# Kernel tuning notes

Hardware: AMD Instinct MI355X
Metric: run time of the kernel (lower is better)

## Reference

```python
import jax, jax.numpy as jnp
import numpy as np

B, S, W, MODES, NUM, NLAYERS = 32, 8192, 128, 16, 8, 4
LG = 8192 + 40 - 1  # szie + len - 1 (Gabor filter length)
PI = float(np.pi)


def setup_inputs() -> dict:
    key = jax.random.key(0)
    ks = jax.random.split(key, 10)
    scale = 1.0 / (W * W)
    return {
        "x": jax.random.normal(ks[0], (B, S, 1), jnp.float32),
        "w1_re": scale * jax.random.uniform(ks[1], (NLAYERS, W, W, MODES), jnp.float32),
        "w1_im": scale * jax.random.uniform(ks[2], (NLAYERS, W, W, MODES), jnp.float32),
        "gamma": jnp.tile(jnp.linspace(0.01, 0.02, NUM, dtype=jnp.float32)[None], (NLAYERS, 1)),
        "fwhm": jnp.tile(jnp.linspace(0.001, 0.002, NUM, dtype=jnp.float32)[None], (NLAYERS, 1)),
        "w2": jax.random.uniform(ks[3], (NLAYERS, NUM), jnp.float32),
        "cw": jax.random.normal(ks[4], (NLAYERS, W, W), jnp.float32) / np.sqrt(W),
        "cb": jnp.zeros((NLAYERS, W), jnp.float32),
        "fc0_w": jax.random.normal(ks[5], (W, 2), jnp.float32) / np.sqrt(2.0),
        "fc0_b": jnp.zeros((W,), jnp.float32),
        "fc1_w": jax.random.normal(ks[6], (128, W), jnp.float32) / np.sqrt(W),
        "fc1_b": jnp.zeros((128,), jnp.float32),
        "fc2_w": jax.random.normal(ks[7], (1, 128), jnp.float32) / np.sqrt(128.0),
        "fc2_b": jnp.zeros((1,), jnp.float32),
    }


def _spectral_conv(h, w_re, w_im, gamma, fwhm, w2):
    # h: [B, C, S] real. w_re/w_im: [C, C, MODES]. gamma/fwhm/w2: [NUM].
    u = jnp.linspace(-0.5, 0.5, LG, dtype=h.dtype)                      # [LG]
    t1 = (gamma * PI / (fwhm + 1e-5))[:, None]                          # [NUM,1]
    gab = jnp.exp(-(t1 ** 2) * (u[None, :] - fwhm[:, None]) ** 2)       # [NUM,LG]
    gab = jnp.fft.ifftshift(gab, axes=-1)[:, :MODES]                     # [NUM,MODES]
    # weights2 is a scalar per latent kernel -> fold the num-reduction into an
    # effective per-mode Gabor weight (exact same math as the repeated einsum + sum).
    g_eff = jnp.einsum("k,km->m", w2, gab)                               # [MODES]
    w1 = (w_re + 1j * w_im) * g_eff[None, None, :]                       # [C,C,MODES] complex
    xf = jnp.fft.rfft(h)                                                 # [B,C,F], F=S//2+1
    out_m = jnp.einsum("bim,iom->bom", xf[..., :MODES], w1)              # [B,C,MODES]
    out = jnp.zeros(xf.shape, dtype=xf.dtype).at[..., :MODES].set(out_m)
    return jnp.fft.irfft(out, n=h.shape[-1])                             # [B,C,S]


def reference(x, w1_re, w1_im, gamma, fwhm, w2, cw, cb, fc0_w, fc0_b, fc1_w, fc1_b, fc2_w, fc2_b):
    b, s, _ = x.shape
    grid = jnp.broadcast_to(jnp.linspace(0.0, 1.0, s, dtype=x.dtype)[None, :, None], (b, s, 1))
    h = jnp.concatenate([x, grid], axis=-1)                              # [B,S,2]
    h = h @ fc0_w.T + fc0_b                                              # [B,S,W]
    h = jnp.transpose(h, (0, 2, 1))                                      # [B,W,S]
    for l in range(NLAYERS):
        x1 = _spectral_conv(h, w1_re[l], w1_im[l], gamma[l], fwhm[l], w2[l])
        x2 = jnp.einsum("oi,bis->bos", cw[l], h) + cb[l][None, :, None]  # 1x1 conv
        h = x1 + x2
        if l < NLAYERS - 1:
            h = jax.nn.gelu(h, approximate=False)
    h = jnp.transpose(h, (0, 2, 1))                                      # [B,S,W]
    h = jax.nn.gelu(h @ fc1_w.T + fc1_b, approximate=False)              # [B,S,128]
    return h @ fc2_w.T + fc2_b                                           # [B,S,1]
```

## Files before the change

### kernel.cpp

```cpp
#include <hip/hip_runtime.h>
#include <hip/hip_fp16.h>

#define BB 32
#define SS 8192
#define CC 128
#define MM 16
#define NUMK 8
#define NL 4

#define TWO_PI 6.2831853071795864769f

typedef _Float16 f16x8 __attribute__((ext_vector_type(8)));
typedef float f32x4 __attribute__((ext_vector_type(4)));

#define MFMA16(a, b, c) __builtin_amdgcn_mfma_f32_16x16x32_f16((a), (b), (c), 0, 0, 0)

__device__ __forceinline__ float gelu_f(float v) {
    float u = 0.7978845608f * fmaf(0.044715f * v * v, v, v);
    float a = fabsf(u);
    float e = __expf(-2.0f * a);
    float th = __fdividef(1.0f - e, 1.0f + e);
    th = copysignf(th, u);
    return 0.5f * v * (1.0f + th);
}

__device__ __align__(256) __half g_trigA[SS * 32];
__device__ __align__(256) __half g_trigD[32 * SS];
__device__ __align__(256) __half g_cwh[NL * CC * CC];
__device__ __align__(256) __half g_fc1h[CC * CC];
__device__ __align__(256) __half g_omh[BB * CC * 32];
__device__ __align__(256) float  g_Xfp[BB * 64 * 32 * CC];
__device__ __align__(256) float  g_Xf[BB * 32 * CC];
__device__ __align__(256) float  g_Xx[BB * MM * 2];
__device__ __align__(256) float  g_Xg[MM * 2];

__global__ __launch_bounds__(256) void k_prep(const float* __restrict__ cw,
                                              const float* __restrict__ fc1_w) {
    int idx = blockIdx.x * 256 + threadIdx.x;
    if (idx < NL * CC * CC) g_cwh[idx] = __float2half(cw[idx]);
    if (idx < CC * CC)      g_fc1h[idx] = __float2half(fc1_w[idx]);
}

__global__ __launch_bounds__(256) void k_trig() {
    int s = blockIdx.x * 256 + threadIdx.x;
    for (int m = 0; m < MM; m++) {
        int ms = (m * s) & (SS - 1);
        float th = (float)ms * (TWO_PI / (float)SS);
        float sn, cs;
        sincosf(th, &sn, &cs);
        g_trigA[s * 32 + m]        = __float2half(cs);
        g_trigA[s * 32 + 16 + m]   = __float2half(sn);
        g_trigD[m * SS + s]        = __float2half(cs);
        g_trigD[(16 + m) * SS + s] = __float2half(-sn);
    }
}

__global__ __launch_bounds__(256) void k_dftx(const float* __restrict__ x) {
    __shared__ float red[4][MM][2];
    int blk = blockIdx.x;
    int t = threadIdx.x;
    int lane = t & 63;
    int wv = t >> 6;

    float accR[MM], accI[MM], cr[MM], ci[MM], pc[MM], ps[MM];
#pragma unroll
    for (int m = 0; m < MM; m++) {
        float sn, cs;
        sincosf((TWO_PI / (float)SS) * (float)(m * t), &sn, &cs);
        cr[m] = cs; ci[m] = -sn;
        sincosf((TWO_PI * 256.0f / (float)SS) * (float)m, &sn, &cs);
        pc[m] = cs; ps[m] = -sn;
        accR[m] = 0.f; accI[m] = 0.f;
    }
    for (int k = 0; k < 32; k++) {
        int s = t + (k << 8);
        float v = (blk < BB) ? x[(blk << 13) + s] : (float)s * (1.0f / 8191.0f);
#pragma unroll
        for (int m = 0; m < MM; m++) {
            accR[m] = fmaf(v, cr[m], accR[m]);
            accI[m] = fmaf(v, ci[m], accI[m]);
            float nc = cr[m] * pc[m] - ci[m] * ps[m];
            float ns = cr[m] * ps[m] + ci[m] * pc[m];
            cr[m] = nc; ci[m] = ns;
        }
    }
#pragma unroll
    for (int m = 0; m < MM; m++) {
#pragma unroll
        for (int off = 32; off > 0; off >>= 1) {
            accR[m] += __shfl_xor(accR[m], off, 64);
            accI[m] += __shfl_xor(accI[m], off, 64);
        }
        if (lane == 0) { red[wv][m][0] = accR[m]; red[wv][m][1] = accI[m]; }
    }
    __syncthreads();
    if (t < MM * 2) {
        int m = t >> 1, p = t & 1;
        float s = red[0][m][p] + red[1][m][p] + red[2][m][p] + red[3][m][p];
        if (blk < BB) g_Xx[(blk << 5) + (m << 1) + p] = s;
        else          g_Xg[(m << 1) + p] = s;
    }
}

__global__ __launch_bounds__(256) void k_xf0(const float* __restrict__ fc0_w,
                                             const float* __restrict__ fc0_b) {
    int n = blockIdx.x * 256 + threadIdx.x;
    int i = n & 127, m2 = (n >> 7) & 31, b = n >> 12;
    int m = m2 & 15, p = m2 >> 4;
    float xv = g_Xx[(b << 5) + (m << 1) + p];
    float gv = g_Xg[(m << 1) + p];
    float v = fc0_w[2 * i] * xv + fc0_w[2 * i + 1] * gv;
    if (p == 0 && m == 0) v += (float)SS * fc0_b[i];
    g_Xf[(b << 12) + (m2 << 7) + i] = v;
}

__global__ __launch_bounds__(256) void k_fc0(const float* __restrict__ x,
                                             const float* __restrict__ fc0_w,
                                             const float* __restrict__ fc0_b,
                                             __half2* __restrict__ h2) {
    int idx = blockIdx.x * 256 + threadIdx.x;
    int w2i = idx & 63;
    int s = (idx >> 6) & (SS - 1);
    int b = idx >> 19;
    int w = w2i * 2;
    float g = (float)s * (1.0f / (float)(SS - 1));
    float xv = x[(b << 13) + s];
    float v0 = fmaf(fc0_w[2 * w], xv, fmaf(fc0_w[2 * w + 1], g, fc0_b[w]));
    float v1 = fmaf(fc0_w[2 * w + 2], xv, fmaf(fc0_w[2 * w + 3], g, fc0_b[w + 1]));
    h2[idx] = __floats2half2_rn(v0, v1);
}

__global__ __launch_bounds__(256) void k_red2() {
    int n = blockIdx.x * 256 + threadIdx.x;
    int i = n & 127, m2 = (n >> 7) & 31, b = n >> 12;
    const float* p = g_Xfp + (((b << 6) << 5) + (m2 << 7)) + i;
    float s = 0.f;
#pragma unroll 8
    for (int t = 0; t < 64; t++) s += p[t << 12];
    g_Xf[(b << 12) + (m2 << 7) + i] = s;
}

__global__ __launch_bounds__(256) void k_mix(const float* __restrict__ w1_re,
                                             const float* __restrict__ w1_im,
                                             const float* __restrict__ gamma,
                                             const float* __restrict__ fwhm,
                                             const float* __restrict__ w2,
                                             const float* __restrict__ cb, int l) {
    __shared__ float geff[MM];
    int t = threadIdx.x;
    if (t < MM) {
        float g = 0.f;
        for (int k = 0; k < NUMK; k++) {
            float fw = fwhm[l * NUMK + k];
            float t1 = gamma[l * NUMK + k] * 3.14159265358979f / (fw + 1e-5f);
            float u = (float)t * (1.0f / 8230.0f) - fw;
            g = fmaf(w2[l * NUMK + k], expf(-t1 * t1 * u * u), g);
        }
        geff[t] = g;
    }
    __syncthreads();

    int n = blockIdx.x * 256 + t;
    int m = n & 15, o = (n >> 4) & 127, b = n >> 11;
    const float* xr = g_Xf + (b << 12) + (m << 7);
    const float* xi = g_Xf + (b << 12) + ((16 + m) << 7);
    const float* wr = w1_re + (l << 18) + (o << 4) + m;
    const float* wi = w1_im + (l << 18) + (o << 4) + m;
    float orr = 0.f, oii = 0.f;
    for (int i = 0; i < CC; i++) {
        float xrv = xr[i], xiv = xi[i];
        float wrv = wr[i << 11], wiv = wi[i << 11];
        orr = fmaf(xrv, wrv, orr); orr = fmaf(-xiv, wiv, orr);
        oii = fmaf(xrv, wiv, oii); oii = fmaf(xiv, wrv, oii);
    }
    float sc = geff[m] * (2.0f / (float)SS) * ((m == 0) ? 0.5f : 1.0f);
    float base = (m == 0) ? cb[l * CC + o] : 0.0f;
    g_omh[(b << 12) + (o << 5) + m]      = __float2half(orr * sc + base);
    g_omh[(b << 12) + (o << 5) + 16 + m] = __float2half(-oii * sc);
}

#define GEMM_STEP(KS, HA, HB)                                                       \
    _Pragma("unroll")                                                               \
    for (int af = 0; af < 8; af++) {                                                \
        int row = (af << 4) + lr;                                                   \
        const f16x8 av = *(const f16x8*)(ldsA + (row << 8) +                        \
                          ((((KS << 2) + lg) ^ (row & 7)) << 4));                   \
        acc[af][0] = MFMA16(av, HA, acc[af][0]);                                    \
        acc[af][1] = MFMA16(av, HB, acc[af][1]);                                    \
    }

#define LOAD_HF(S0X)                                                                \
    {                                                                               \
        int hr = (((b << 13) + (S0X) + (wid << 5) + lr) << 8) + (lg << 4);          \
        hf0 = *(const f16x8*)(h_c + hr);                                            \
        hf1 = *(const f16x8*)(h_c + hr + (16 << 8));                                \
        hf2 = *(const f16x8*)(h_c + hr + (1 << 6));                                 \
        hf3 = *(const f16x8*)(h_c + hr + (16 << 8) + (1 << 6));                     \
        hf4 = *(const f16x8*)(h_c + hr + (2 << 6));                                 \
        hf5 = *(const f16x8*)(h_c + hr + (16 << 8) + (2 << 6));                     \
        hf6 = *(const f16x8*)(h_c + hr + (3 << 6));                                 \
        hf7 = *(const f16x8*)(h_c + hr + (16 << 8) + (3 << 6));                     \
    }

template <int TAIL>
__global__ __launch_bounds__(256, 2) void k_layer(__half* __restrict__ h, int l) {
    __shared__ __align__(16) char smem[TAIL ? 73728 : 40960];
    char* ldsA = smem;
    char* ldsO = smem + 32768;
    char* ldsS = smem + (TAIL ? 40960 : 0);
    int bi = blockIdx.x;
    int b = bi >> 4, grp = bi & 15;
    int Sg = grp << 9;
    int t = threadIdx.x;
    int wid = __builtin_amdgcn_readfirstlane(t >> 6);
    int l6 = t & 63, lr = l6 & 15, lg = l6 >> 4;
    const char* h_c = (const char*)h;
    char* hw = (char*)h;
    const char* cw_c = (const char*)(g_cwh + l * CC * CC);
    const char* om_c = (const char*)(g_omh + (b << 12));
    const char* ta_c = (const char*)g_trigA;
    const char* td_c = (const char*)g_trigD;
    char* strip = ldsS + (wid << 13);

#pragma unroll
    for (int k = 0; k < 8; k++) {
        int c = (k << 8) + t;
        f16x8 v = *(const f16x8*)(cw_c + (c << 4));
        int row = c >> 4, c16 = c & 15;
        *(f16x8*)(ldsA + (row << 8) + ((c16 ^ (row & 7)) << 4)) = v;
    }
#pragma unroll
    for (int k = 0; k < 2; k++) {
        int c = (k << 8) + t;
        f16x8 v = *(const f16x8*)(om_c + (c << 4));
        int row = c >> 2, c4 = c & 3;
        *(f16x8*)(ldsO + (row << 6) + ((c4 ^ (row & 3)) << 4)) = v;
    }
    f16x8 hf0, hf1, hf2, hf3, hf4, hf5, hf6, hf7;
    LOAD_HF(Sg)
    __syncthreads();

    f32x4 dacc[8][2];
    if (TAIL) {
#pragma unroll
        for (int af = 0; af < 8; af++) {
            dacc[af][0] = (f32x4){0.f, 0.f, 0.f, 0.f};
            dacc[af][1] = (f32x4){0.f, 0.f, 0.f, 0.f};
        }
    }

    for (int ti = 0; ti < 4; ti++) {
        int S0 = Sg + (ti << 7);
        f32x4 acc[8][2];
#pragma unroll
        for (int af = 0; af < 8; af++) {
            acc[af][0] = (f32x4){0.f, 0.f, 0.f, 0.f};
            acc[af][1] = (f32x4){0.f, 0.f, 0.f, 0.f};
        }
        __builtin_amdgcn_s_setprio(1);
        GEMM_STEP(0, hf0, hf1)
        GEMM_STEP(1, hf2, hf3)
        GEMM_STEP(2, hf4, hf5)
        GEMM_STEP(3, hf6, hf7)
        {
            int tr2 = ((S0 + (wid << 5) + lr) << 6) + (lg << 4);
            f16x8 tf0 = *(const f16x8*)(ta_c + tr2);
            f16x8 tf1 = *(const f16x8*)(ta_c + tr2 + (16 << 6));
#pragma unroll
            for (int af = 0; af < 8; af++) {
                int row = (af << 4) + lr;
                const f16x8 ov = *(const f16x8*)(ldsO + (row << 6) + ((lg ^ (row & 3)) << 4));
                acc[af][0] = MFMA16(ov, tf0, acc[af][0]);
                acc[af][1] = MFMA16(ov, tf1, acc[af][1]);
            }
        }
        __builtin_amdgcn_s_setprio(0);
        {
            int tn = (ti < 3) ? ti + 1 : ti;
            int S0n = Sg + (tn << 7);
            LOAD_HF(S0n)
        }
#pragma unroll
        for (int bf = 0; bf < 2; bf++) {
            int s_w = (bf << 4) + lr;
            int s = S0 + (wid << 5) + s_w;
#pragma unroll
            for (int af = 0; af < 8; af++) {
                int o0 = (af << 4) + (lg << 2);
                float v0 = acc[af][bf][0], v1 = acc[af][bf][1];
                float v2 = acc[af][bf][2], v3 = acc[af][bf][3];
                if (TAIL) { v0 = gelu_f(v0); v1 = gelu_f(v1); v2 = gelu_f(v2); v3 = gelu_f(v3); }
                union { __half2 q[2]; unsigned long long u; } pk;
                pk.q[0] = __floats2half2_rn(v0, v1);
                pk.q[1] = __floats2half2_rn(v2, v3);
                *(unsigned long long*)(hw + (((b << 13) + s) << 8) + (o0 << 1)) = pk.u;
                if (TAIL) {
                    int byte = (s_w << 8) + ((o0 << 1) ^ ((s_w & 15) << 4));
                    *(unsigned long long*)(strip + byte) = pk.u;
                }
            }
        }
        if (TAIL) {
            asm volatile("s_waitcnt lgkmcnt(0)" ::: "memory");
            __builtin_amdgcn_sched_barrier(0);
            int sgl = S0 + (wid << 5) + (lg << 3);
            f16x8 a0 = *(const f16x8*)(td_c + (((lr << 13) + sgl) << 1));
            f16x8 a1 = *(const f16x8*)(td_c + ((((16 + lr) << 13) + sgl) << 1));
#pragma unroll
            for (int af = 0; af < 8; af++) {
                int o = (af << 4) + lr;
                union { unsigned int u[4]; f16x8 v; } bb;
#pragma unroll
                for (int p = 0; p < 4; p++) {
                    int s0 = (lg << 3) + 2 * p, s1 = s0 + 1;
                    unsigned int lo = *(const unsigned short*)
                        (strip + (s0 << 8) + ((o << 1) ^ ((s0 & 15) << 4)));
                    unsigned int hi = *(const unsigned short*)
                        (strip + (s1 << 8) + ((o << 1) ^ ((s1 & 15) << 4)));
                    bb.u[p] = lo | (hi << 16);
                }
                dacc[af][0] = MFMA16(a0, bb.v, dacc[af][0]);
                dacc[af][1] = MFMA16(a1, bb.v, dacc[af][1]);
            }
        }
    }
    if (TAIL) {
        float* xp = g_Xfp + (((b << 6) + (grp << 2) + wid) << 12);
#pragma unroll
        for (int af = 0; af < 8; af++)
#pragma unroll
            for (int mh = 0; mh < 2; mh++)
#pragma unroll
                for (int reg = 0; reg < 4; reg++) {
                    int m2 = (mh << 4) + (lg << 2) + reg;
                    int o = (af << 4) + lr;
                    xp[(m2 << 7) + o] = dacc[af][mh][reg];
                }
    }
}

__global__ __launch_bounds__(256) void k_head(const __half* __restrict__ h,
                                              const float* __restrict__ fc1_b,
                                              const float* __restrict__ fc2_w,
                                              const float* __restrict__ fc2_b,
                                              float* __restrict__ out) {
    __shared__ __align__(16) char smem[32768];
    char* ldsA = smem;
    int bi = blockIdx.x;
    int b = bi >> 4, grp = bi & 15;
    int Sg = grp << 9;
    int t = threadIdx.x;
    int wid = __builtin_amdgcn_readfirstlane(t >> 6);
    int l6 = t & 63, lr = l6 & 15, lg = l6 >> 4;
    const char* h_c = (const char*)h;
    const char* f1_c = (const char*)g_fc1h;

#pragma unroll
    for (int k = 0; k < 8; k++) {
        int c = (k << 8) + t;
        f16x8 v = *(const f16x8*)(f1_c + (c << 4));
        int row = c >> 4, c16 = c & 15;
        *(f16x8*)(ldsA + (row << 8) + ((c16 ^ (row & 7)) << 4)) = v;
    }
    f16x8 hf0, hf1, hf2, hf3, hf4, hf5, hf6, hf7;
    LOAD_HF(Sg)
    __syncthreads();

    float f2b = fc2_b[0];
    for (int ti = 0; ti < 4; ti++) {
        int S0 = Sg + (ti << 7);
        f32x4 acc[8][2];
#pragma unroll
        for (int af = 0; af < 8; af++) {
            acc[af][0] = (f32x4){0.f, 0.f, 0.f, 0.f};
            acc[af][1] = (f32x4){0.f, 0.f, 0.f, 0.f};
        }
        __builtin_amdgcn_s_setprio(1);
        GEMM_STEP(0, hf0, hf1)
        GEMM_STEP(1, hf2, hf3)
        GEMM_STEP(2, hf4, hf5)
        GEMM_STEP(3, hf6, hf7)
        __builtin_amdgcn_s_setprio(0);
        {
            int tn = (ti < 3) ? ti + 1 : ti;
            int S0n = Sg + (tn << 7);
            LOAD_HF(S0n)
        }
        float p[2] = {0.f, 0.f};
#pragma unroll
        for (int af = 0; af < 8; af++) {
            float4 fb = *(const float4*)(fc1_b + (af << 4) + (lg << 2));
            float4 f2 = *(const float4*)(fc2_w + (af << 4) + (lg << 2));
#pragma unroll
            for (int bf = 0; bf < 2; bf++) {
                float v0 = gelu_f(acc[af][bf][0] + fb.x);
                float v1 = gelu_f(acc[af][bf][1] + fb.y);
                float v2 = gelu_f(acc[af][bf][2] + fb.z);
                float v3 = gelu_f(acc[af][bf][3] + fb.w);
                p[bf] += f2.x * v0 + f2.y * v1 + f2.z * v2 + f2.w * v3;
            }
        }
#pragma unroll
        for (int bf = 0; bf < 2; bf++) {
            float v = p[bf];
            v += __shfl_xor(v, 16, 64);
            v += __shfl_xor(v, 32, 64);
            if (lg == 0) out[(b << 13) + S0 + (wid << 5) + (bf << 4) + lr] = v + f2b;
        }
    }
}

extern "C" void kernel_launch(void* const* d_in, const int* in_sizes, int n_in,
                              void* d_out, int out_size, void* d_ws, size_t ws_size,
                              hipStream_t stream) {
    const float* x      = (const float*)d_in[0];
    const float* w1_re  = (const float*)d_in[1];
    const float* w1_im  = (const float*)d_in[2];
    const float* gamma  = (const float*)d_in[3];
    const float* fwhm   = (const float*)d_in[4];
    const float* w2     = (const float*)d_in[5];
    const float* cw     = (const float*)d_in[6];
    const float* cb     = (const float*)d_in[7];
    const float* fc0_w  = (const float*)d_in[8];
    const float* fc0_b  = (const float*)d_in[9];
    const float* fc1_w  = (const float*)d_in[10];
    const float* fc1_b  = (const float*)d_in[11];
    const float* fc2_w  = (const float*)d_in[12];
    const float* fc2_b  = (const float*)d_in[13];
    float* out = (float*)d_out;

    __half* h = (__half*)d_ws;

    k_prep<<<dim3(256), dim3(256), 0, stream>>>(cw, fc1_w);
    k_trig<<<dim3(32), dim3(256), 0, stream>>>();
    k_dftx<<<dim3(33), dim3(256), 0, stream>>>(x);
    k_xf0<<<dim3(512), dim3(256), 0, stream>>>(fc0_w, fc0_b);
    k_fc0<<<dim3(65536), dim3(256), 0, stream>>>(x, fc0_w, fc0_b, (__half2*)h);
    for (int l = 0; l < NL; l++) {
        k_mix<<<dim3(256), dim3(256), 0, stream>>>(w1_re, w1_im, gamma, fwhm, w2, cb, l);
        if (l < NL - 1) {
            k_layer<1><<<dim3(512), dim3(256), 0, stream>>>(h, l);
            k_red2<<<dim3(512), dim3(256), 0, stream>>>();
        } else {
            k_layer<0><<<dim3(512), dim3(256), 0, stream>>>(h, l);
        }
    }
    k_head<<<dim3(512), dim3(256), 0, stream>>>(h, fc1_b, fc2_w, fc2_b, out);
}
```

Before: 344.9 us.

## Halve per-block sequence span, shrink LDS, and store DFT partials in fp16

Each block of k_layer and k_head now covers 256 sequence positions instead of 512, so grids double to 1024 blocks. LDS use drops because the omega tile is read straight from global memory and the strip buffer is smaller, which allows three blocks per CU. The forward-DFT accumulation is done per 16-row half-strip with accumulators reset per tile. Per-tile partial spectra are written as fp16 into a buffer four times larger, and k_red2 sums 256 partials instead of 64. This trades more reduction traffic and lower precision in the partials for more parallelism and occupancy.

```diff
diff --git a/kernel.cpp b/kernel.cpp
--- a/kernel.cpp
+++ b/kernel.cpp
@@ -29,7 +29,7 @@
 __device__ __align__(256) __half g_cwh[NL * CC * CC];
 __device__ __align__(256) __half g_fc1h[CC * CC];
 __device__ __align__(256) __half g_omh[BB * CC * 32];
-__device__ __align__(256) float  g_Xfp[BB * 64 * 32 * CC];
+__device__ __align__(256) __half g_Xfp[BB * 256 * 32 * CC];
 __device__ __align__(256) float  g_Xf[BB * 32 * CC];
 __device__ __align__(256) float  g_Xx[BB * MM * 2];
 __device__ __align__(256) float  g_Xg[MM * 2];
@@ -133,10 +133,10 @@
 __global__ __launch_bounds__(256) void k_red2() {
     int n = blockIdx.x * 256 + threadIdx.x;
     int i = n & 127, m2 = (n >> 7) & 31, b = n >> 12;
-    const float* p = g_Xfp + (((b << 6) << 5) + (m2 << 7)) + i;
+    const __half* p = g_Xfp + (((long)b << 20)) + (m2 << 7) + i;
     float s = 0.f;
 #pragma unroll 8
-    for (int t = 0; t < 64; t++) s += p[t << 12];
+    for (int t = 0; t < 256; t++) s += __half2float(p[t << 12]);
     g_Xf[(b << 12) + (m2 << 7) + i] = s;
 }
 
@@ -203,14 +203,12 @@
     }
 
 template <int TAIL>
-__global__ __launch_bounds__(256, 2) void k_layer(__half* __restrict__ h, int l) {
-    __shared__ __align__(16) char smem[TAIL ? 73728 : 40960];
+__global__ __launch_bounds__(256, 3) void k_layer(__half* __restrict__ h, int l) {
+    __shared__ __align__(16) char smem[TAIL ? 49152 : 32768];
     char* ldsA = smem;
-    char* ldsO = smem + 32768;
-    char* ldsS = smem + (TAIL ? 40960 : 0);
     int bi = blockIdx.x;
-    int b = bi >> 4, grp = bi & 15;
-    int Sg = grp << 9;
+    int b = bi >> 5, grp = bi & 31;
+    int Sg = grp << 8;
     int t = threadIdx.x;
     int wid = __builtin_amdgcn_readfirstlane(t >> 6);
     int l6 = t & 63, lr = l6 & 15, lg = l6 >> 4;
@@ -220,7 +218,7 @@
     const char* om_c = (const char*)(g_omh + (b << 12));
     const char* ta_c = (const char*)g_trigA;
     const char* td_c = (const char*)g_trigD;
-    char* strip = ldsS + (wid << 13);
+    char* strip = smem + 32768 + (wid << 12);
 
 #pragma unroll
     for (int k = 0; k < 8; k++) {
@@ -229,27 +227,11 @@
         int row = c >> 4, c16 = c & 15;
         *(f16x8*)(ldsA + (row << 8) + ((c16 ^ (row & 7)) << 4)) = v;
     }
-#pragma unroll
-    for (int k = 0; k < 2; k++) {
-        int c = (k << 8) + t;
-        f16x8 v = *(const f16x8*)(om_c + (c << 4));
-        int row = c >> 2, c4 = c & 3;
-        *(f16x8*)(ldsO + (row << 6) + ((c4 ^ (row & 3)) << 4)) = v;
-    }
     f16x8 hf0, hf1, hf2, hf3, hf4, hf5, hf6, hf7;
     LOAD_HF(Sg)
     __syncthreads();
 
-    f32x4 dacc[8][2];
-    if (TAIL) {
-#pragma unroll
-        for (int af = 0; af < 8; af++) {
-            dacc[af][0] = (f32x4){0.f, 0.f, 0.f, 0.f};
-            dacc[af][1] = (f32x4){0.f, 0.f, 0.f, 0.f};
-        }
-    }
-
-    for (int ti = 0; ti < 4; ti++) {
+    for (int ti = 0; ti < 2; ti++) {
         int S0 = Sg + (ti << 7);
         f32x4 acc[8][2];
 #pragma unroll
@@ -268,22 +250,25 @@
             f16x8 tf1 = *(const f16x8*)(ta_c + tr2 + (16 << 6));
 #pragma unroll
             for (int af = 0; af < 8; af++) {
-                int row = (af << 4) + lr;
-                const f16x8 ov = *(const f16x8*)(ldsO + (row << 6) + ((lg ^ (row & 3)) << 4));
+                f16x8 ov = *(const f16x8*)(om_c + (((af << 4) + lr) << 6) + (lg << 4));
                 acc[af][0] = MFMA16(ov, tf0, acc[af][0]);
                 acc[af][1] = MFMA16(ov, tf1, acc[af][1]);
             }
         }
         __builtin_amdgcn_s_setprio(0);
-        {
-            int tn = (ti < 3) ? ti + 1 : ti;
-            int S0n = Sg + (tn << 7);
-            LOAD_HF(S0n)
+        if (ti == 0) { LOAD_HF(Sg + 128) }
+
+        f32x4 dacc[8][2];
+        if (TAIL) {
+#pragma unroll
+            for (int af = 0; af < 8; af++) {
+                dacc[af][0] = (f32x4){0.f, 0.f, 0.f, 0.f};
+                dacc[af][1] = (f32x4){0.f, 0.f, 0.f, 0.f};
+            }
         }
 #pragma unroll
         for (int bf = 0; bf < 2; bf++) {
-            int s_w = (bf << 4) + lr;
-            int s = S0 + (wid << 5) + s_w;
+            int s = S0 + (wid << 5) + (bf << 4) + lr;
 #pragma unroll
             for (int af = 0; af < 8; af++) {
                 int o0 = (af << 4) + (lg << 2);
@@ -295,60 +280,65 @@
                 pk.q[1] = __floats2half2_rn(v2, v3);
                 *(unsigned long long*)(hw + (((b << 13) + s) << 8) + (o0 << 1)) = pk.u;
                 if (TAIL) {
-                    int byte = (s_w << 8) + ((o0 << 1) ^ ((s_w & 15) << 4));
+                    int byte = (lr << 8) + ((o0 << 1) ^ (lr << 4));
                     *(unsigned long long*)(strip + byte) = pk.u;
                 }
             }
+            if (TAIL) {
+                asm volatile("s_waitcnt lgkmcnt(0)" ::: "memory");
+                __builtin_amdgcn_sched_barrier(0);
+                int lgr = lg & 1;
+                int sgl = S0 + (wid << 5) + (bf << 4) + (lgr << 3);
+                f16x8 a0 = {}; f16x8 a1 = {};
+                if (lg < 2) {
+                    a0 = *(const f16x8*)(td_c + (((lr << 13) + sgl) << 1));
+                    a1 = *(const f16x8*)(td_c + ((((16 + lr) << 13) + sgl) << 1));
+                }
+#pragma unroll
+                for (int af = 0; af < 8; af++) {
+                    int o = (af << 4) + lr;
+                    union { unsigned int u[4]; f16x8 v; } bb;
+#pragma unroll
+                    for (int p = 0; p < 4; p++) {
+                        int s0 = (lgr << 3) + 2 * p, s1 = s0 + 1;
+                        unsigned int lo = *(const unsigned short*)
+                            (strip + (s0 << 8) + ((o << 1) ^ (s0 << 4)));
+                        unsigned int hi = *(const unsigned short*)
+                            (strip + (s1 << 8) + ((o << 1) ^ (s1 << 4)));
+                        bb.u[p] = lo | (hi << 16);
+                    }
+                    dacc[af][0] = MFMA16(a0, bb.v, dacc[af][0]);
+                    dacc[af][1] = MFMA16(a1, bb.v, dacc[af][1]);
+                }
+                __builtin_amdgcn_sched_barrier(0);
+            }
         }
         if (TAIL) {
-            asm volatile("s_waitcnt lgkmcnt(0)" ::: "memory");
-            __builtin_amdgcn_sched_barrier(0);
-            int sgl = S0 + (wid << 5) + (lg << 3);
-            f16x8 a0 = *(const f16x8*)(td_c + (((lr << 13) + sgl) << 1));
-            f16x8 a1 = *(const f16x8*)(td_c + ((((16 + lr) << 13) + sgl) << 1));
-#pragma unroll
-            for (int af = 0; af < 8; af++) {
-                int o = (af << 4) + lr;
-                union { unsigned int u[4]; f16x8 v; } bb;
-#pragma unroll
-                for (int p = 0; p < 4; p++) {
-                    int s0 = (lg << 3) + 2 * p, s1 = s0 + 1;
-                    unsigned int lo = *(const unsigned short*)
-                        (strip + (s0 << 8) + ((o << 1) ^ ((s0 & 15) << 4)));
-                    unsigned int hi = *(const unsigned short*)
-                        (strip + (s1 << 8) + ((o << 1) ^ ((s1 & 15) << 4)));
-                    bb.u[p] = lo | (hi << 16);
-                }
-                dacc[af][0] = MFMA16(a0, bb.v, dacc[af][0]);
-                dacc[af][1] = MFMA16(a1, bb.v, dacc[af][1]);
-            }
-        }
-    }
-    if (TAIL) {
-        float* xp = g_Xfp + (((b << 6) + (grp << 2) + wid) << 12);
-#pragma unroll
-        for (int af = 0; af < 8; af++)
-#pragma unroll
-            for (int mh = 0; mh < 2; mh++)
-#pragma unroll
-                for (int reg = 0; reg < 4; reg++) {
-                    int m2 = (mh << 4) + (lg << 2) + reg;
-                    int o = (af << 4) + lr;
-                    xp[(m2 << 7) + o] = dacc[af][mh][reg];
-                }
-    }
-}
-
-__global__ __launch_bounds__(256) void k_head(const __half* __restrict__ h,
-                                              const float* __restrict__ fc1_b,
-                                              const float* __restrict__ fc2_w,
-                                              const float* __restrict__ fc2_b,
-                                              float* __restrict__ out) {
+            __half* xp = g_Xfp + (((long)(b << 8) + (((grp << 1) + ti) << 2) + wid) << 12);
+#pragma unroll
+            for (int af = 0; af < 8; af++)
+#pragma unroll
+                for (int mh = 0; mh < 2; mh++)
+#pragma unroll
+                    for (int reg = 0; reg < 4; reg++) {
+                        int m2 = (mh << 4) + (lg << 2) + reg;
+                        int o = (af << 4) + lr;
+                        xp[(m2 << 7) + o] = __float2half(dacc[af][mh][reg]);
+                    }
+        }
+    }
+}
+
+__global__ __launch_bounds__(256, 3) void k_head(const __half* __restrict__ h,
+                                                 const float* __restrict__ fc1_b,
+                                                 const float* __restrict__ fc2_w,
+                                                 const float* __restrict__ fc2_b,
+                                                 float* __restrict__ out) {
     __shared__ __align__(16) char smem[32768];
     char* ldsA = smem;
     int bi = blockIdx.x;
-    int b = bi >> 4, grp = bi & 15;
-    int Sg = grp << 9;
+    int b = bi >> 5, grp = bi & 31;
+    int Sg = grp << 8;
     int t = threadIdx.x;
     int wid = __builtin_amdgcn_readfirstlane(t >> 6);
     int l6 = t & 63, lr = l6 & 15, lg = l6 >> 4;
@@ -367,7 +357,7 @@
     __syncthreads();
 
     float f2b = fc2_b[0];
-    for (int ti = 0; ti < 4; ti++) {
+    for (int ti = 0; ti < 2; ti++) {
         int S0 = Sg + (ti << 7);
         f32x4 acc[8][2];
 #pragma unroll
@@ -381,11 +371,7 @@
         GEMM_STEP(2, hf4, hf5)
         GEMM_STEP(3, hf6, hf7)
         __builtin_amdgcn_s_setprio(0);
-        {
-            int tn = (ti < 3) ? ti + 1 : ti;
-            int S0n = Sg + (tn << 7);
-            LOAD_HF(S0n)
-        }
+        if (ti == 0) { LOAD_HF(Sg + 128) }
         float p[2] = {0.f, 0.f};
 #pragma unroll
         for (int af = 0; af < 8; af++) {
@@ -439,11 +425,11 @@
     for (int l = 0; l < NL; l++) {
         k_mix<<<dim3(256), dim3(256), 0, stream>>>(w1_re, w1_im, gamma, fwhm, w2, cb, l);
         if (l < NL - 1) {
-            k_layer<1><<<dim3(512), dim3(256), 0, stream>>>(h, l);
+            k_layer<1><<<dim3(1024), dim3(256), 0, stream>>>(h, l);
             k_red2<<<dim3(512), dim3(256), 0, stream>>>();
         } else {
-            k_layer<0><<<dim3(512), dim3(256), 0, stream>>>(h, l);
-        }
-    }
-    k_head<<<dim3(512), dim3(256), 0, stream>>>(h, fc1_b, fc2_w, fc2_b, out);
-}
+            k_layer<0><<<dim3(1024), dim3(256), 0, stream>>>(h, l);
+        }
+    }
+    k_head<<<dim3(1024), dim3(256), 0, stream>>>(h, fc1_b, fc2_w, fc2_b, out);
+}
```

New measurement: 837.3 us. 2.43x slower.
